# Optimization experiments

Hardware: AMD Instinct MI355X
Metric: run time of the kernel (lower is better)

The kernel has to match this reference:

```python
import jax, jax.numpy as jnp
import numpy as np

IMAGE_DIM = 224


def setup_inputs() -> dict:
    key = jax.random.key(0)
    k1, k2, k3, k4, k5 = jax.random.split(key, 5)
    N, H, W = 64, IMAGE_DIM, IMAGE_DIM
    im1 = jax.random.normal(k1, (N, 3, H, W), dtype=jnp.float32)
    im2 = jax.random.normal(k2, (N, 3, H, W), dtype=jnp.float32)
    C = jax.random.normal(k3, (N, 2, H, W), dtype=jnp.float32)
    M1 = jax.random.uniform(k4, (N, 1, H, W), dtype=jnp.float32)
    M2 = jax.random.uniform(k5, (N, 1, H, W), dtype=jnp.float32)
    return {"im1": im1, "im2": im2, "C": C, "M1": M1, "M2": M2}


def _grid(dtype):
    # q = [repeat(arange(H), W), tile(arange(W), H)], shape [2, H*W]
    x = jnp.repeat(jnp.arange(IMAGE_DIM), IMAGE_DIM)
    y = jnp.tile(jnp.arange(IMAGE_DIM), IMAGE_DIM)
    return jnp.stack([x, y]).astype(dtype)  # [2, HW]


def _bilinear_sample(imflat, qi):
    # imflat: [N, 3, HW], qi: [N, 2, HW] float coords
    HW = imflat.shape[-1]
    px, py = qi[:, 0], qi[:, 1]  # [N, HW]
    fx, cx = jnp.floor(px), jnp.ceil(px)
    fy, cy = jnp.floor(py), jnp.ceil(py)

    def gather_pixel(nx, ny):
        # weight = prod over axes of (1 - |point - neighbor|)
        w = (1.0 - jnp.abs(px - nx)) * (1.0 - jnp.abs(py - ny))  # [N, HW]
        ind = (nx + IMAGE_DIM * ny).astype(jnp.int32)
        ind = jnp.clip(ind, 0, HW - 1)  # guard against out-of-range neighbors
        pix = jnp.take_along_axis(imflat, ind[:, None, :], axis=2)  # [N, 3, HW]
        return w[:, None, :] * pix

    return (gather_pixel(fx, fy) + gather_pixel(cx, fy)
            + gather_pixel(fx, cy) + gather_pixel(cy * 0 + cx, cy))


def reference(im1, im2, C, M1, M2):
    N, ch, H, W = im1.shape
    HW = H * W
    q = _grid(im1.dtype)[None]              # [1, 2, HW]
    Cflat = C.reshape(N, 2, HW)
    a = _bilinear_sample(im1.reshape(N, ch, HW), q + Cflat).reshape(N, ch, H, W) * M1
    b = _bilinear_sample(im2.reshape(N, ch, HW), q - Cflat).reshape(N, ch, H, W) * M2
    return a + b
```

## Files before the change

kernel.cpp:

```cpp
#include <hip/hip_runtime.h>

#define IMG 224
#define HW (IMG * IMG)
#define TILE 32
#define PAD 4
#define REG (TILE + 2 * PAD)
#define RST (REG + 1)
#define TSZ (REG * RST)

__global__ __launch_bounds__(256, 4) void vm_kernel(
    const float* __restrict__ im1, const float* __restrict__ im2,
    const float* __restrict__ C, const float* __restrict__ M1,
    const float* __restrict__ M2, float* __restrict__ out)
{
    __shared__ float smem[6 * TSZ];

    const int n    = blockIdx.y;
    const int tile = blockIdx.x;
    const int x0   = (tile / 7) * TILE;
    const int y0   = (tile % 7) * TILE;
    const int t    = threadIdx.x;
    const int xlo  = x0 - PAD;
    const int ylo  = y0 - PAD;

    const float* i1n = im1 + (size_t)n * 3 * HW;
    const float* i2n = im2 + (size_t)n * 3 * HW;
    const float* Cn  = C  + (size_t)n * 2 * HW;
    const float* M1n = M1 + (size_t)n * HW;
    const float* M2n = M2 + (size_t)n * HW;

#pragma unroll
    for (int k = 0; k < 7; ++k) {
        int e = t + 256 * k;
        if (e < REG * REG) {
            int r  = e / REG;
            int c  = e - r * REG;
            int gi = (xlo + c) + IMG * (ylo + r);
            gi = min(max(gi, 0), HW - 1);
            int ls = r * RST + c;
#pragma unroll
            for (int ch = 0; ch < 3; ++ch) {
                smem[ch * TSZ + ls]       = i1n[ch * HW + gi];
                smem[(3 + ch) * TSZ + ls] = i2n[ch * HW + gi];
            }
        }
    }

    float c0[4], c1[4], m1v[4], m2v[4];
#pragma unroll
    for (int j = 0; j < 4; ++j) {
        int idx = t + 256 * j;
        int tx  = idx >> 5;
        int ty  = idx & 31;
        int p   = (x0 + tx) * IMG + (y0 + ty);
        c0[j]  = Cn[p];
        c1[j]  = Cn[HW + p];
        m1v[j] = M1n[p];
        m2v[j] = M2n[p];
    }

    __syncthreads();

    float* on = out + (size_t)n * 3 * HW;
#pragma unroll
    for (int j = 0; j < 4; ++j) {
        int idx = t + 256 * j;
        int tx  = idx >> 5;
        int ty  = idx & 31;
        int p   = (x0 + tx) * IMG + (y0 + ty);
        float xf = (float)(x0 + tx);
        float yf = (float)(y0 + ty);

        int   oA[4], oB[4];
        float wA[4], wB[4];
        int fa, fb;
        {
            float px = xf + c0[j], py = yf + c1[j];
            float fx = floorf(px), cx = ceilf(px);
            float fy = floorf(py), cy = ceilf(py);
            float wfx = 1.0f - (px - fx), wcx = 1.0f - (cx - px);
            float wfy = 1.0f - (py - fy), wcy = 1.0f - (cy - py);
            wA[0] = wfx * wfy; wA[1] = wcx * wfy;
            wA[2] = wfx * wcy; wA[3] = wcx * wcy;
            int gx0 = (int)fx, gy0 = (int)fy;
            int dx = (int)cx - gx0, dy = (int)cy - gy0;
            int q0 = gx0 - xlo, r0 = gy0 - ylo;
            int o  = r0 * RST + q0;
            oA[0] = o;            oA[1] = o + dx;
            oA[2] = o + dy * RST; oA[3] = o + dx + dy * RST;
            fa = __all((q0 >= 0) & (q0 + dx <= REG - 1) &
                       (r0 >= 0) & (r0 + dy <= REG - 1));
        }
        {
            float px = xf - c0[j], py = yf - c1[j];
            float fx = floorf(px), cx = ceilf(px);
            float fy = floorf(py), cy = ceilf(py);
            float wfx = 1.0f - (px - fx), wcx = 1.0f - (cx - px);
            float wfy = 1.0f - (py - fy), wcy = 1.0f - (cy - py);
            wB[0] = wfx * wfy; wB[1] = wcx * wfy;
            wB[2] = wfx * wcy; wB[3] = wcx * wcy;
            int gx0 = (int)fx, gy0 = (int)fy;
            int dx = (int)cx - gx0, dy = (int)cy - gy0;
            int q0 = gx0 - xlo, r0 = gy0 - ylo;
            int o  = r0 * RST + q0;
            oB[0] = o;            oB[1] = o + dx;
            oB[2] = o + dy * RST; oB[3] = o + dx + dy * RST;
            fb = __all((q0 >= 0) & (q0 + dx <= REG - 1) &
                       (r0 >= 0) & (r0 + dy <= REG - 1));
        }

        float res[3];
        if (fa) {
#pragma unroll
            for (int ch = 0; ch < 3; ++ch) {
                const float* T = smem + ch * TSZ;
                res[ch] = m1v[j] *
                    (wA[0] * T[oA[0]] + wA[1] * T[oA[1]] +
                     wA[2] * T[oA[2]] + wA[3] * T[oA[3]]);
            }
        } else {
            float px = xf + c0[j], py = yf + c1[j];
            float fx = floorf(px), cx = ceilf(px);
            float fy = floorf(py), cy = ceilf(py);
            int i0 = min(max((int)fx + IMG * (int)fy, 0), HW - 1);
            int i1 = min(max((int)cx + IMG * (int)fy, 0), HW - 1);
            int i2 = min(max((int)fx + IMG * (int)cy, 0), HW - 1);
            int i3 = min(max((int)cx + IMG * (int)cy, 0), HW - 1);
#pragma unroll
            for (int ch = 0; ch < 3; ++ch) {
                const float* pa = i1n + ch * HW;
                res[ch] = m1v[j] *
                    (wA[0] * pa[i0] + wA[1] * pa[i1] +
                     wA[2] * pa[i2] + wA[3] * pa[i3]);
            }
        }
        if (fb) {
#pragma unroll
            for (int ch = 0; ch < 3; ++ch) {
                const float* T = smem + (3 + ch) * TSZ;
                res[ch] += m2v[j] *
                    (wB[0] * T[oB[0]] + wB[1] * T[oB[1]] +
                     wB[2] * T[oB[2]] + wB[3] * T[oB[3]]);
            }
        } else {
            float px = xf - c0[j], py = yf - c1[j];
            float fx = floorf(px), cx = ceilf(px);
            float fy = floorf(py), cy = ceilf(py);
            int i0 = min(max((int)fx + IMG * (int)fy, 0), HW - 1);
            int i1 = min(max((int)cx + IMG * (int)fy, 0), HW - 1);
            int i2 = min(max((int)fx + IMG * (int)cy, 0), HW - 1);
            int i3 = min(max((int)cx + IMG * (int)cy, 0), HW - 1);
#pragma unroll
            for (int ch = 0; ch < 3; ++ch) {
                const float* pb = i2n + ch * HW;
                res[ch] += m2v[j] *
                    (wB[0] * pb[i0] + wB[1] * pb[i1] +
                     wB[2] * pb[i2] + wB[3] * pb[i3]);
            }
        }

#pragma unroll
        for (int ch = 0; ch < 3; ++ch)
            on[ch * HW + p] = res[ch];
    }
}

extern "C" void kernel_launch(void* const* d_in, const int* in_sizes, int n_in,
                              void* d_out, int out_size, void* d_ws, size_t ws_size,
                              hipStream_t stream) {
    const float* im1 = (const float*)d_in[0];
    const float* im2 = (const float*)d_in[1];
    const float* C   = (const float*)d_in[2];
    const float* M1  = (const float*)d_in[3];
    const float* M2  = (const float*)d_in[4];
    float* out = (float*)d_out;
    dim3 grid(49, 64);
    vm_kernel<<<grid, 256, 0, stream>>>(im1, im2, C, M1, M2, out);
}
```

Baseline: 172.3 us.

## Vectorize tile loads and stores, pack channels as float2 in LDS

```diff
diff --git a/kernel.cpp b/kernel.cpp
--- a/kernel.cpp
+++ b/kernel.cpp
@@ -5,15 +5,18 @@
 #define TILE 32
 #define PAD 4
 #define REG (TILE + 2 * PAD)
-#define RST (REG + 1)
-#define TSZ (REG * RST)
+#define RSA 41
+#define TABA (REG * RSA)
+#define RSB 44
+#define TABB (REG * RSB)
 
 __global__ __launch_bounds__(256, 4) void vm_kernel(
     const float* __restrict__ im1, const float* __restrict__ im2,
     const float* __restrict__ C, const float* __restrict__ M1,
     const float* __restrict__ M2, float* __restrict__ out)
 {
-    __shared__ float smem[6 * TSZ];
+    __shared__ float2 tabA[2 * TABA];
+    __shared__ float  tabB[2 * TABB];
 
     const int n    = blockIdx.y;
     const int tile = blockIdx.x;
@@ -22,6 +25,7 @@
     const int t    = threadIdx.x;
     const int xlo  = x0 - PAD;
     const int ylo  = y0 - PAD;
+    const int gbase = xlo + IMG * ylo;
 
     const float* i1n = im1 + (size_t)n * 3 * HW;
     const float* i2n = im2 + (size_t)n * 3 * HW;
@@ -30,139 +34,144 @@
     const float* M2n = M2 + (size_t)n * HW;
 
 #pragma unroll
-    for (int k = 0; k < 7; ++k) {
-        int e = t + 256 * k;
-        if (e < REG * REG) {
-            int r  = e / REG;
-            int c  = e - r * REG;
-            int gi = (xlo + c) + IMG * (ylo + r);
-            gi = min(max(gi, 0), HW - 1);
-            int ls = r * RST + c;
+    for (int img = 0; img < 2; ++img) {
+        const float* src = img ? i2n : i1n;
+        float2* TA = tabA + img * TABA;
+        float*  TB = tabB + img * TABB;
 #pragma unroll
-            for (int ch = 0; ch < 3; ++ch) {
-                smem[ch * TSZ + ls]       = i1n[ch * HW + gi];
-                smem[(3 + ch) * TSZ + ls] = i2n[ch * HW + gi];
+        for (int k = 0; k < 2; ++k) {
+            int e = t + 256 * k;
+            if (e < 400) {
+                int r = e / 10, s = e - r * 10;
+                int gi = gbase + IMG * r + 4 * s;
+                float4 a, b, c;
+                if (gi >= 0 && gi <= HW - 4) {
+                    a = *(const float4*)(src + gi);
+                    b = *(const float4*)(src + HW + gi);
+                    c = *(const float4*)(src + 2 * HW + gi);
+                } else {
+#pragma unroll
+                    for (int i = 0; i < 4; ++i) {
+                        int g = min(max(gi + i, 0), HW - 1);
+                        ((float*)&a)[i] = src[g];
+                        ((float*)&b)[i] = src[HW + g];
+                        ((float*)&c)[i] = src[2 * HW + g];
+                    }
+                }
+                float2* dA = TA + r * RSA + 4 * s;
+                dA[0] = make_float2(a.x, b.x);
+                dA[1] = make_float2(a.y, b.y);
+                dA[2] = make_float2(a.z, b.z);
+                dA[3] = make_float2(a.w, b.w);
+                *(float4*)(TB + r * RSB + 4 * s) = c;
             }
         }
     }
 
-    float c0[4], c1[4], m1v[4], m2v[4];
-#pragma unroll
-    for (int j = 0; j < 4; ++j) {
-        int idx = t + 256 * j;
-        int tx  = idx >> 5;
-        int ty  = idx & 31;
-        int p   = (x0 + tx) * IMG + (y0 + ty);
-        c0[j]  = Cn[p];
-        c1[j]  = Cn[HW + p];
-        m1v[j] = M1n[p];
-        m2v[j] = M2n[p];
-    }
+    const int tx  = t >> 3;
+    const int ty0 = (t & 7) * 4;
+    const int p   = (x0 + tx) * IMG + (y0 + ty0);
+
+    const float4 c0v = *(const float4*)(Cn + p);
+    const float4 c1v = *(const float4*)(Cn + HW + p);
+    const float4 m1v = *(const float4*)(M1n + p);
+    const float4 m2v = *(const float4*)(M2n + p);
 
     __syncthreads();
 
-    float* on = out + (size_t)n * 3 * HW;
+    const float xf = (float)(x0 + tx);
+    float acc0[4], acc1[4], acc2[4];
+
 #pragma unroll
-    for (int j = 0; j < 4; ++j) {
-        int idx = t + 256 * j;
-        int tx  = idx >> 5;
-        int ty  = idx & 31;
-        int p   = (x0 + tx) * IMG + (y0 + ty);
-        float xf = (float)(x0 + tx);
-        float yf = (float)(y0 + ty);
+    for (int i = 0; i < 4; ++i) {
+        const float yf  = (float)(y0 + ty0 + i);
+        const float cc0 = ((const float*)&c0v)[i];
+        const float cc1 = ((const float*)&c1v)[i];
+        const float m1i = ((const float*)&m1v)[i];
+        const float m2i = ((const float*)&m2v)[i];
+        float r0c, r1c, r2c;
 
-        int   oA[4], oB[4];
-        float wA[4], wB[4];
-        int fa, fb;
         {
-            float px = xf + c0[j], py = yf + c1[j];
+            float px = xf + cc0, py = yf + cc1;
             float fx = floorf(px), cx = ceilf(px);
             float fy = floorf(py), cy = ceilf(py);
             float wfx = 1.0f - (px - fx), wcx = 1.0f - (cx - px);
             float wfy = 1.0f - (py - fy), wcy = 1.0f - (cy - py);
-            wA[0] = wfx * wfy; wA[1] = wcx * wfy;
-            wA[2] = wfx * wcy; wA[3] = wcx * wcy;
+            float w0 = wfx * wfy, w1 = wcx * wfy;
+            float w2 = wfx * wcy, w3 = wcx * wcy;
             int gx0 = (int)fx, gy0 = (int)fy;
             int dx = (int)cx - gx0, dy = (int)cy - gy0;
             int q0 = gx0 - xlo, r0 = gy0 - ylo;
-            int o  = r0 * RST + q0;
-            oA[0] = o;            oA[1] = o + dx;
-            oA[2] = o + dy * RST; oA[3] = o + dx + dy * RST;
-            fa = __all((q0 >= 0) & (q0 + dx <= REG - 1) &
-                       (r0 >= 0) & (r0 + dy <= REG - 1));
+            int in = (q0 >= 0) & (q0 + dx <= REG - 1) &
+                     (r0 >= 0) & (r0 + dy <= REG - 1);
+            if (__all(in)) {
+                int oA = r0 * RSA + q0;
+                int oB = r0 * RSB + q0;
+                float2 a0 = tabA[oA],            a1 = tabA[oA + dx];
+                float2 a2 = tabA[oA + dy * RSA], a3 = tabA[oA + dx + dy * RSA];
+                float  b0 = tabB[oB],            b1 = tabB[oB + dx];
+                float  b2 = tabB[oB + dy * RSB], b3 = tabB[oB + dx + dy * RSB];
+                r0c = m1i * (w0 * a0.x + w1 * a1.x + w2 * a2.x + w3 * a3.x);
+                r1c = m1i * (w0 * a0.y + w1 * a1.y + w2 * a2.y + w3 * a3.y);
+                r2c = m1i * (w0 * b0   + w1 * b1   + w2 * b2   + w3 * b3);
+            } else {
+                int i0 = min(max(gx0      + IMG * gy0,        0), HW - 1);
+                int i1 = min(max(gx0 + dx + IMG * gy0,        0), HW - 1);
+                int i2 = min(max(gx0      + IMG * (gy0 + dy), 0), HW - 1);
+                int i3 = min(max(gx0 + dx + IMG * (gy0 + dy), 0), HW - 1);
+                r0c = m1i * (w0 * i1n[i0] + w1 * i1n[i1] +
+                             w2 * i1n[i2] + w3 * i1n[i3]);
+                r1c = m1i * (w0 * i1n[HW + i0] + w1 * i1n[HW + i1] +
+                             w2 * i1n[HW + i2] + w3 * i1n[HW + i3]);
+                r2c = m1i * (w0 * i1n[2 * HW + i0] + w1 * i1n[2 * HW + i1] +
+                             w2 * i1n[2 * HW + i2] + w3 * i1n[2 * HW + i3]);
+            }
         }
         {
-            float px = xf - c0[j], py = yf - c1[j];
+            float px = xf - cc0, py = yf - cc1;
             float fx = floorf(px), cx = ceilf(px);
             float fy = floorf(py), cy = ceilf(py);
             float wfx = 1.0f - (px - fx), wcx = 1.0f - (cx - px);
             float wfy = 1.0f - (py - fy), wcy = 1.0f - (cy - py);
-            wB[0] = wfx * wfy; wB[1] = wcx * wfy;
-            wB[2] = wfx * wcy; wB[3] = wcx * wcy;
+            float w0 = wfx * wfy, w1 = wcx * wfy;
+            float w2 = wfx * wcy, w3 = wcx * wcy;
             int gx0 = (int)fx, gy0 = (int)fy;
             int dx = (int)cx - gx0, dy = (int)cy - gy0;
             int q0 = gx0 - xlo, r0 = gy0 - ylo;
-            int o  = r0 * RST + q0;
-            oB[0] = o;            oB[1] = o + dx;
-            oB[2] = o + dy * RST; oB[3] = o + dx + dy * RST;
-            fb = __all((q0 >= 0) & (q0 + dx <= REG - 1) &
-                       (r0 >= 0) & (r0 + dy <= REG - 1));
-        }
-
-        float res[3];
-        if (fa) {
-#pragma unroll
-            for (int ch = 0; ch < 3; ++ch) {
-                const float* T = smem + ch * TSZ;
-                res[ch] = m1v[j] *
-                    (wA[0] * T[oA[0]] + wA[1] * T[oA[1]] +
-                     wA[2] * T[oA[2]] + wA[3] * T[oA[3]]);
-            }
-        } else {
-            float px = xf + c0[j], py = yf + c1[j];
-            float fx = floorf(px), cx = ceilf(px);
-            float fy = floorf(py), cy = ceilf(py);
-            int i0 = min(max((int)fx + IMG * (int)fy, 0), HW - 1);
-            int i1 = min(max((int)cx + IMG * (int)fy, 0), HW - 1);
-            int i2 = min(max((int)fx + IMG * (int)cy, 0), HW - 1);
-            int i3 = min(max((int)cx + IMG * (int)cy, 0), HW - 1);
-#pragma unroll
-            for (int ch = 0; ch < 3; ++ch) {
-                const float* pa = i1n + ch * HW;
-                res[ch] = m1v[j] *
-                    (wA[0] * pa[i0] + wA[1] * pa[i1] +
-                     wA[2] * pa[i2] + wA[3] * pa[i3]);
+            int in = (q0 >= 0) & (q0 + dx <= REG - 1) &
+                     (r0 >= 0) & (r0 + dy <= REG - 1);
+            if (__all(in)) {
+                const float2* TA = tabA + TABA;
+                const float*  TB = tabB + TABB;
+                int oA = r0 * RSA + q0;
+                int oB = r0 * RSB + q0;
+                float2 a0 = TA[oA],            a1 = TA[oA + dx];
+                float2 a2 = TA[oA + dy * RSA], a3 = TA[oA + dx + dy * RSA];
+                float  b0 = TB[oB],            b1 = TB[oB + dx];
+                float  b2 = TB[oB + dy * RSB], b3 = TB[oB + dx + dy * RSB];
+                r0c += m2i * (w0 * a0.x + w1 * a1.x + w2 * a2.x + w3 * a3.x);
+                r1c += m2i * (w0 * a0.y + w1 * a1.y + w2 * a2.y + w3 * a3.y);
+                r2c += m2i * (w0 * b0   + w1 * b1   + w2 * b2   + w3 * b3);
+            } else {
+                int i0 = min(max(gx0      + IMG * gy0,        0), HW - 1);
+                int i1 = min(max(gx0 + dx + IMG * gy0,        0), HW - 1);
+                int i2 = min(max(gx0      + IMG * (gy0 + dy), 0), HW - 1);
+                int i3 = min(max(gx0 + dx + IMG * (gy0 + dy), 0), HW - 1);
+                r0c += m2i * (w0 * i2n[i0] + w1 * i2n[i1] +
+                              w2 * i2n[i2] + w3 * i2n[i3]);
+                r1c += m2i * (w0 * i2n[HW + i0] + w1 * i2n[HW + i1] +
+                              w2 * i2n[HW + i2] + w3 * i2n[HW + i3]);
+                r2c += m2i * (w0 * i2n[2 * HW + i0] + w1 * i2n[2 * HW + i1] +
+                              w2 * i2n[2 * HW + i2] + w3 * i2n[2 * HW + i3]);
             }
         }
-        if (fb) {
-#pragma unroll
-            for (int ch = 0; ch < 3; ++ch) {
-                const float* T = smem + (3 + ch) * TSZ;
-                res[ch] += m2v[j] *
-                    (wB[0] * T[oB[0]] + wB[1] * T[oB[1]] +
-                     wB[2] * T[oB[2]] + wB[3] * T[oB[3]]);
-            }
-        } else {
-            float px = xf - c0[j], py = yf - c1[j];
-            float fx = floorf(px), cx = ceilf(px);
-            float fy = floorf(py), cy = ceilf(py);
-            int i0 = min(max((int)fx + IMG * (int)fy, 0), HW - 1);
-            int i1 = min(max((int)cx + IMG * (int)fy, 0), HW - 1);
-            int i2 = min(max((int)fx + IMG * (int)cy, 0), HW - 1);
-            int i3 = min(max((int)cx + IMG * (int)cy, 0), HW - 1);
-#pragma unroll
-            for (int ch = 0; ch < 3; ++ch) {
-                const float* pb = i2n + ch * HW;
-                res[ch] += m2v[j] *
-                    (wB[0] * pb[i0] + wB[1] * pb[i1] +
-                     wB[2] * pb[i2] + wB[3] * pb[i3]);
-            }
-        }
+        acc0[i] = r0c; acc1[i] = r1c; acc2[i] = r2c;
+    }
 
-#pragma unroll
-        for (int ch = 0; ch < 3; ++ch)
-            on[ch * HW + p] = res[ch];
-    }
+    float* on = out + (size_t)n * 3 * HW;
+    *(float4*)(on + p)          = make_float4(acc0[0], acc0[1], acc0[2], acc0[3]);
+    *(float4*)(on + HW + p)     = make_float4(acc1[0], acc1[1], acc1[2], acc1[3]);
+    *(float4*)(on + 2 * HW + p) = make_float4(acc2[0], acc2[1], acc2[2], acc2[3]);
 }
 
 extern "C" void kernel_launch(void* const* d_in, const int* in_sizes, int n_in,
```

Measured after the change: 171.2 us. About the same (-0.6%).
